# Performance work log

Hardware: AMD Instinct MI355X
Metric: run time of the kernel (lower is better)

The kernel has to match this reference:

```python
import jax, jax.numpy as jnp
import numpy as np

EMBED_DIM = 1024
N_HEADS = 16


def setup_inputs() -> dict:
    key = jax.random.key(0)
    k1, k2, k3 = jax.random.split(key, 3)
    B, T, C = 4, 2048, EMBED_DIM
    x0 = jax.random.normal(k1, (B, T, C), dtype=jnp.float32)
    # Linear weights stored as (in, out) so y = x @ W, matching torch Linear math.
    w_attn = jax.random.normal(k2, (C, 3 * C), dtype=jnp.float32) * (1.0 / np.sqrt(C))
    w_proj = jax.random.normal(k3, (C, C), dtype=jnp.float32) * (1.0 / np.sqrt(C))
    return {"x0": x0, "w_attn": w_attn, "w_proj": w_proj}


def reference(x0, w_attn, w_proj):
    B, T, C = x0.shape
    H = N_HEADS
    D = C // H  # head dim
    qkv = x0 @ w_attn                      # [B, T, 3C]
    q, k, v = jnp.split(qkv, 3, axis=-1)
    # [B, T, C] -> [B, H, T, D]
    q = q.reshape(B, T, H, D).transpose(0, 2, 1, 3)
    k = k.reshape(B, T, H, D).transpose(0, 2, 1, 3)
    v = v.reshape(B, T, H, D).transpose(0, 2, 1, 3)
    scale = 1.0 / np.sqrt(D)
    attn = jnp.einsum('bhqd,bhkd->bhqk', q, k) * scale  # [B, H, T, T]
    causal = jnp.tril(jnp.ones((T, T), dtype=bool))
    attn = jnp.where(causal[None, None, :, :], attn, -jnp.inf)
    attn = jax.nn.softmax(attn, axis=-1)
    y = jnp.einsum('bhqk,bhkd->bhqd', attn, v)           # [B, H, T, D]
    y = y.transpose(0, 2, 1, 3).reshape(B, T, C)
    return y @ w_proj
```

## Files before the change

kernel.cpp:

```cpp
#include <hip/hip_runtime.h>

#define TSEQ 2048
#define NB 4
#define NH 16
#define HD 64
#define CEMB 1024
#define MROWS (NB*TSEQ)

typedef _Float16 half8 __attribute__((ext_vector_type(8)));
typedef _Float16 half4_t __attribute__((ext_vector_type(4)));
typedef float floatx4 __attribute__((ext_vector_type(4)));

__device__ __forceinline__ floatx4 mfma16x32(half8 a, half8 b, floatx4 c) {
    return __builtin_amdgcn_mfma_f32_16x16x32_f16(a, b, c, 0, 0, 0);
}

__device__ __forceinline__ void async16(const _Float16* g, _Float16* l) {
    __builtin_amdgcn_global_load_lds((const __attribute__((address_space(1))) void*)g,
                                     (__attribute__((address_space(3))) void*)l, 16, 0, 0);
}

__global__ __launch_bounds__(256) void cvt_fp32_fp16(const float* __restrict__ in,
                                                     _Float16* __restrict__ out) {
    size_t i = ((size_t)blockIdx.x * 256 + threadIdx.x) * 8;
    float4 a = *(const float4*)(in + i);
    float4 b = *(const float4*)(in + i + 4);
    half8 h;
    h[0] = (_Float16)a.x; h[1] = (_Float16)a.y; h[2] = (_Float16)a.z; h[3] = (_Float16)a.w;
    h[4] = (_Float16)b.x; h[5] = (_Float16)b.y; h[6] = (_Float16)b.z; h[7] = (_Float16)b.w;
    *(half8*)(out + i) = h;
}

__global__ __launch_bounds__(256) void transpose_cvt(const float* __restrict__ in,
                                                     _Float16* __restrict__ out,
                                                     int R, int Ccols) {
    __shared__ float tile[32][33];
    int bx = blockIdx.x;
    int by = blockIdx.y;
    int tx = threadIdx.x, ty = threadIdx.y;
    int x = bx * 32 + tx;
#pragma unroll
    for (int i = 0; i < 32; i += 8) {
        int y = by * 32 + ty + i;
        tile[ty + i][tx] = in[(size_t)y * Ccols + x];
    }
    __syncthreads();
#pragma unroll
    for (int i = 0; i < 32; i += 8) {
        int oc = bx * 32 + ty + i;
        int orow = by * 32 + tx;
        out[(size_t)oc * R + orow] = (_Float16)tile[tx][ty + i];
    }
}

template<int MODE>
__global__ __launch_bounds__(512, 2) void gemm_nt8(const _Float16* __restrict__ A,
                                                   const _Float16* __restrict__ Bt,
                                                   float* __restrict__ Cf,
                                                   _Float16* __restrict__ Ch,
                                                   _Float16* __restrict__ VTh,
                                                   int N, int K) {
    __shared__ __align__(16) _Float16 As[4][128 * 32];
    __shared__ __align__(16) _Float16 Bs[4][256 * 32];

    const int tid = threadIdx.x;
    const int wv = tid >> 6, lane = tid & 63;
    const int wm = wv >> 2, wn = wv & 3;
    const int l16 = lane & 15, quad = lane >> 4;

    const int pid = blockIdx.x + gridDim.x * blockIdx.y;
    const int nn = gridDim.y;
    const int pig = 8 * nn;
    const int gid = pid / pig;
    const int rem = pid - gid * pig;
    const int bm = gid * 8 + (rem & 7);
    const int bn = rem >> 3;

    const int rA = tid >> 2;
    const int kA = ((tid & 3) ^ ((rA >> 1) & 3)) * 8;
    const _Float16* Ag  = A  + (size_t)(bm * 128 + rA) * K + kA;
    const _Float16* Bg0 = Bt + (size_t)(bn * 256 + rA) * K + kA;
    const _Float16* Bg1 = Bg0 + (size_t)128 * K;

    auto stage = [&](int slot, int ss) {
        async16(Ag  + ss * 32, &As[slot][wv * 512]);
        async16(Bg0 + ss * 32, &Bs[slot][wv * 512]);
        async16(Bg1 + ss * 32, &Bs[slot][4096 + wv * 512]);
    };

    const floatx4 zero = {0.f, 0.f, 0.f, 0.f};
    floatx4 acc[4][4];
#pragma unroll
    for (int i = 0; i < 4; i++)
#pragma unroll
        for (int j = 0; j < 4; j++) acc[i][j] = zero;

    const int sw2 = (quad ^ ((l16 >> 1) & 3)) * 8;
    const int offA = (wm * 64 + l16) * 32 + sw2;
    const int offB = (wn * 64 + l16) * 32 + sw2;

    stage(0, 0); stage(1, 1); stage(2, 2);
    asm volatile("s_waitcnt vmcnt(6)\n\ts_barrier" ::: "memory");

    const int NS = K >> 5;
    for (int it = 0; it < NS / 4; ++it) {
#pragma unroll
        for (int p = 0; p < 4; ++p) {
            const int s = it * 4 + p;
            half8 af[4], bf[4];
#pragma unroll
            for (int i = 0; i < 4; i++) af[i] = *(const half8*)&As[p][offA + i * 512];
#pragma unroll
            for (int j = 0; j < 4; j++) bf[j] = *(const half8*)&Bs[p][offB + j * 512];
            if (s + 3 < NS) stage((p + 3) & 3, s + 3);
            asm volatile("s_barrier" ::: "memory");
            __builtin_amdgcn_sched_barrier(0);
            __builtin_amdgcn_s_setprio(1);
#pragma unroll
            for (int i = 0; i < 4; i++)
#pragma unroll
                for (int j = 0; j < 4; j++)
                    acc[i][j] = mfma16x32(af[i], bf[j], acc[i][j]);
            __builtin_amdgcn_s_setprio(0);
            __builtin_amdgcn_sched_barrier(0);
            asm volatile("s_waitcnt vmcnt(6)\n\ts_barrier" ::: "memory");
        }
    }

    if (MODE == 1) {
#pragma unroll
        for (int i = 0; i < 4; i++) {
            int row = bm * 128 + wm * 64 + i * 16 + quad * 4;
#pragma unroll
            for (int j = 0; j < 4; j++) {
                int col = bn * 256 + wn * 64 + j * 16 + l16;
#pragma unroll
                for (int r = 0; r < 4; r++)
                    Cf[(size_t)(row + r) * N + col] = acc[i][j][r];
            }
        }
    } else {
        const int which = bn >> 2;
        if (which < 2) {
#pragma unroll
            for (int j = 0; j < 4; j++) {
                int n = bn * 256 + wn * 64 + j * 16 + l16;
                int c = n & 1023, h = c >> 6, d = c & 63;
                _Float16* dst = Ch + (size_t)which * ((size_t)MROWS * CEMB)
                                   + (size_t)h * (TSEQ * HD) + d;
#pragma unroll
                for (int i = 0; i < 4; i++) {
                    int row = bm * 128 + wm * 64 + i * 16 + quad * 4;
#pragma unroll
                    for (int r = 0; r < 4; r++) {
                        int m = row + r;
                        int b = m >> 11, t = m & 2047;
                        dst[(size_t)b * (NH * TSEQ * HD) + (size_t)t * HD] = (_Float16)acc[i][j][r];
                    }
                }
            }
        } else {
#pragma unroll
            for (int j = 0; j < 4; j++) {
                int n = bn * 256 + wn * 64 + j * 16 + l16;
                int c = n & 1023, h = c >> 6, d = c & 63;
#pragma unroll
                for (int i = 0; i < 4; i++) {
                    int m0 = bm * 128 + wm * 64 + i * 16 + quad * 4;
                    int b = m0 >> 11, t = m0 & 2047;
                    half4_t pk;
#pragma unroll
                    for (int r = 0; r < 4; r++) pk[r] = (_Float16)acc[i][j][r];
                    *(half4_t*)&VTh[(((size_t)(b * NH + h)) * HD + d) * TSEQ + t] = pk;
                }
            }
        }
    }
}

__global__ __launch_bounds__(512, 4) void attn_fwd(const _Float16* __restrict__ Qg,
                                                   const _Float16* __restrict__ Kg,
                                                   const _Float16* __restrict__ VTg,
                                                   _Float16* __restrict__ Y) {
    __shared__ __align__(16) _Float16 Ks[2][4096];
    __shared__ __align__(16) _Float16 Vt[2][4096];

    const int tid = threadIdx.x;
    const int w = tid >> 6, lane = tid & 63;
    const int l16 = lane & 15, quad = lane >> 4;
    const int bh = blockIdx.y;
    const int x = blockIdx.x;
    const int b = bh >> 4, h = bh & 15;
    const int qt = (b < 2) ? x : (7 - x);

    const _Float16* Qb = Qg + (size_t)bh * TSEQ * HD;
    const _Float16* Kb = Kg + (size_t)bh * TSEQ * HD;
    const _Float16* Vb = VTg + (size_t)bh * HD * TSEQ;

    const _Float16 ksc = (_Float16)(0.125f * 1.44269504089f);
    const floatx4 zero = {0.f, 0.f, 0.f, 0.f};

    half8 qf[2][2];
#pragma unroll
    for (int g = 0; g < 2; g++) {
        const _Float16* qrow = Qb + (size_t)(qt * 256 + g * 128 + w * 16 + l16) * HD;
        qf[g][0] = *(const half8*)(qrow + quad * 8);
        qf[g][1] = *(const half8*)(qrow + 32 + quad * 8);
#pragma unroll
        for (int e = 0; e < 8; e++) { qf[g][0][e] *= ksc; qf[g][1][e] *= ksc; }
    }

    floatx4 o[2][4];
#pragma unroll
    for (int g = 0; g < 2; g++)
#pragma unroll
        for (int dt = 0; dt < 4; dt++) o[g][dt] = zero;
    float lsum[2] = {0.f, 0.f};

    const int srow8 = lane >> 3;
    const int scol8 = ((lane & 7) ^ (lane >> 3)) * 8;

    auto stage = [&](int bf, int kt2) {
        const int row = w * 8 + srow8;
        async16(Kb + (size_t)(kt2 * 64 + row) * HD + scol8, &Ks[bf][w * 512]);
        async16(Vb + (size_t)row * TSEQ + kt2 * 64 + scol8, &Vt[bf][w * 512]);
    };

    const int kmax = 4 * qt + 3;
    stage(0, 0);
    int buf = 0;
    for (int kt = 0; kt <= kmax; ++kt) {
        __syncthreads();
        if (kt < kmax) stage(buf ^ 1, kt + 1);

        half8 kf0[4], kf1[4];
#pragma unroll
        for (int nj = 0; nj < 4; nj++) {
            const int rb = (nj * 16 + l16) * 64;
            kf0[nj] = *(const half8*)&Ks[buf][rb + ((quad ^ (l16 & 7)) * 8)];
            kf1[nj] = *(const half8*)&Ks[buf][rb + (((quad ^ 4) ^ (l16 & 7)) * 8)];
        }

        const bool doA = (kt <= 4 * qt + 1);
        half8 pf[2][2];
#pragma unroll
        for (int g = 0; g < 2; g++) {
            if (g == 0 && !doA) continue;
            floatx4 st[4];
#pragma unroll
            for (int nj = 0; nj < 4; nj++) {
                floatx4 t = mfma16x32(kf0[nj], qf[g][0], zero);
                st[nj] = mfma16x32(kf1[nj], qf[g][1], t);
            }
            if (kt * 64 + 63 > qt * 256 + g * 128 + w * 16) {
                const int klim = qt * 256 + g * 128 + w * 16 + l16 - kt * 64;
#pragma unroll
                for (int nj = 0; nj < 4; nj++)
#pragma unroll
                    for (int r = 0; r < 4; r++) {
                        int key = nj * 16 + quad * 4 + r;
                        if (key > klim) st[nj][r] = -1e30f;
                    }
            }
#pragma unroll
            for (int nj = 0; nj < 4; nj++)
#pragma unroll
                for (int r = 0; r < 4; r++) {
                    float p = __builtin_amdgcn_exp2f(st[nj][r]);
                    lsum[g] += p;
                    pf[g][nj >> 1][(nj & 1) * 4 + r] = (_Float16)p;
                }
        }

#pragma unroll
        for (int u = 0; u < 2; u++) {
#pragma unroll
            for (int dt = 0; dt < 4; dt++) {
                const int rb = (dt * 16 + l16) * 64;
                const int g0 = u * 4 + (quad >> 1);
                const int sub = (quad & 1) * 4;
                half4_t lo = *(const half4_t*)&Vt[buf][rb + ((g0 ^ (l16 & 7)) * 8 + sub)];
                half4_t hi = *(const half4_t*)&Vt[buf][rb + (((g0 + 2) ^ (l16 & 7)) * 8 + sub)];
                half8 vf;
                vf[0] = lo[0]; vf[1] = lo[1]; vf[2] = lo[2]; vf[3] = lo[3];
                vf[4] = hi[0]; vf[5] = hi[1]; vf[6] = hi[2]; vf[7] = hi[3];
                if (doA) o[0][dt] = mfma16x32(pf[0][u], vf, o[0][dt]);
                o[1][dt] = mfma16x32(pf[1][u], vf, o[1][dt]);
            }
        }
        buf ^= 1;
    }

#pragma unroll
    for (int g = 0; g < 2; g++) {
        float lt = lsum[g];
        lt += __shfl_xor(lt, 16);
        lt += __shfl_xor(lt, 32);
        float linv[4];
#pragma unroll
        for (int r = 0; r < 4; r++) linv[r] = 1.0f / __shfl(lt, quad * 4 + r);
#pragma unroll
        for (int dt = 0; dt < 4; dt++)
#pragma unroll
            for (int r = 0; r < 4; r++) {
                int q = qt * 256 + g * 128 + w * 16 + quad * 4 + r;
                int d = dt * 16 + l16;
                Y[((size_t)(b * TSEQ + q)) * CEMB + h * HD + d] = (_Float16)(o[g][dt][r] * linv[r]);
            }
    }
}

extern "C" void kernel_launch(void* const* d_in, const int* in_sizes, int n_in,
                              void* d_out, int out_size, void* d_ws, size_t ws_size,
                              hipStream_t stream) {
    const float* x0     = (const float*)d_in[0];
    const float* w_attn = (const float*)d_in[1];
    const float* w_proj = (const float*)d_in[2];
    float* out = (float*)d_out;

    _Float16* xh  = (_Float16*)d_ws;
    _Float16* wqt = xh  + (size_t)MROWS * CEMB;
    _Float16* wpt = wqt + (size_t)3 * CEMB * CEMB;
    _Float16* qh  = wpt + (size_t)CEMB * CEMB;
    _Float16* kh  = qh  + (size_t)MROWS * CEMB;
    _Float16* vt  = kh  + (size_t)MROWS * CEMB;
    _Float16* yh  = vt  + (size_t)MROWS * CEMB;

    cvt_fp32_fp16<<<(MROWS * CEMB) / (256 * 8), 256, 0, stream>>>(x0, xh);
    transpose_cvt<<<dim3(3 * CEMB / 32, CEMB / 32), dim3(32, 8), 0, stream>>>(w_attn, wqt, CEMB, 3 * CEMB);
    transpose_cvt<<<dim3(CEMB / 32, CEMB / 32), dim3(32, 8), 0, stream>>>(w_proj, wpt, CEMB, CEMB);

    gemm_nt8<0><<<dim3(MROWS / 128, 3 * CEMB / 256), 512, 0, stream>>>(xh, wqt, nullptr, qh, vt, 3 * CEMB, CEMB);
    attn_fwd<<<dim3(TSEQ / 256, NB * NH), 512, 0, stream>>>(qh, kh, vt, yh);
    gemm_nt8<1><<<dim3(MROWS / 128, CEMB / 256), 512, 0, stream>>>(yh, wpt, out, nullptr, nullptr, CEMB, CEMB);
}
```

Baseline: 242.6 us.

## Double-buffer GEMM register fragments and deepen LDS prefetch to four stages

Restructures the GEMM main loop so LDS-to-register fragment loads for the next k-step are issued before the MFMAs of the current step, using two register fragment buffers. Global-to-LDS async staging now runs four slots ahead, and one of the two barriers per step is removed. The loop trip count is hardcoded to 7 outer iterations plus an epilogue, which assumes K equals 1024. This raises register pressure and breaks if K changes. The tighter waitcnt and barrier placement needs care, because the slot being overwritten must no longer be read by other waves.

```diff
diff --git a/kernel.cpp b/kernel.cpp
--- a/kernel.cpp
+++ b/kernel.cpp
@@ -99,33 +99,49 @@
     const int offA = (wm * 64 + l16) * 32 + sw2;
     const int offB = (wn * 64 + l16) * 32 + sw2;
 
-    stage(0, 0); stage(1, 1); stage(2, 2);
+    half8 fa[2][4], fb[2][4];
+
+#define LDF(d, slot)                                                         \
+    do {                                                                     \
+        _Pragma("unroll") for (int i_ = 0; i_ < 4; i_++)                     \
+            fa[d][i_] = *(const half8*)&As[slot][offA + i_ * 512];           \
+        _Pragma("unroll") for (int j_ = 0; j_ < 4; j_++)                     \
+            fb[d][j_] = *(const half8*)&Bs[slot][offB + j_ * 512];           \
+    } while (0)
+
+#define MM(d)                                                                \
+    do {                                                                     \
+        __builtin_amdgcn_s_setprio(1);                                       \
+        _Pragma("unroll") for (int i_ = 0; i_ < 4; i_++)                     \
+            _Pragma("unroll") for (int j_ = 0; j_ < 4; j_++)                 \
+                acc[i_][j_] = mfma16x32(fa[d][i_], fb[d][j_], acc[i_][j_]);  \
+        __builtin_amdgcn_s_setprio(0);                                       \
+    } while (0)
+
+    stage(0, 0); stage(1, 1); stage(2, 2); stage(3, 3);
     asm volatile("s_waitcnt vmcnt(6)\n\ts_barrier" ::: "memory");
-
-    const int NS = K >> 5;
-    for (int it = 0; it < NS / 4; ++it) {
+    LDF(0, 0);
+
+    for (int it = 0; it < 7; ++it) {
 #pragma unroll
         for (int p = 0; p < 4; ++p) {
-            const int s = it * 4 + p;
-            half8 af[4], bf[4];
-#pragma unroll
-            for (int i = 0; i < 4; i++) af[i] = *(const half8*)&As[p][offA + i * 512];
-#pragma unroll
-            for (int j = 0; j < 4; j++) bf[j] = *(const half8*)&Bs[p][offB + j * 512];
-            if (s + 3 < NS) stage((p + 3) & 3, s + 3);
-            asm volatile("s_barrier" ::: "memory");
+            stage(p, it * 4 + p + 4);
+            LDF((p & 1) ^ 1, (p + 1) & 3);
+            MM(p & 1);
+            asm volatile("s_waitcnt vmcnt(6) lgkmcnt(0)\n\ts_barrier" ::: "memory");
             __builtin_amdgcn_sched_barrier(0);
-            __builtin_amdgcn_s_setprio(1);
-#pragma unroll
-            for (int i = 0; i < 4; i++)
-#pragma unroll
-                for (int j = 0; j < 4; j++)
-                    acc[i][j] = mfma16x32(af[i], bf[j], acc[i][j]);
-            __builtin_amdgcn_s_setprio(0);
-            __builtin_amdgcn_sched_barrier(0);
-            asm volatile("s_waitcnt vmcnt(6)\n\ts_barrier" ::: "memory");
-        }
-    }
+        }
+    }
+    LDF(1, 1); MM(0);
+    asm volatile("s_waitcnt vmcnt(3)\n\ts_barrier" ::: "memory");
+    __builtin_amdgcn_sched_barrier(0);
+    LDF(0, 2); MM(1);
+    asm volatile("s_waitcnt vmcnt(0)\n\ts_barrier" ::: "memory");
+    __builtin_amdgcn_sched_barrier(0);
+    LDF(1, 3); MM(0);
+    MM(1);
+#undef LDF
+#undef MM
 
     if (MODE == 1) {
 #pragma unroll
```

Result: slower. 249.9 us (+3.0%).

## Restructure GEMM to 4 waves with 128x64 per-wave tiles and 3-stage pipeline

Applied to the files above, without the earlier changes.

The GEMM kernel now runs with 256 threads (4 waves) instead of 512. Each wave computes a full 128-row by 64-column output tile (8x4 MFMA accumulators), so each A fragment is reused across more MFMAs. The LDS ring drops from 4 to 3 stages, with a fully unrolled loop hardcoded for K=1024 (32 k-steps), and one barrier per phase instead of two. This raises register pressure and ties the kernel to K=1024.

```diff
diff --git a/kernel.cpp b/kernel.cpp
--- a/kernel.cpp
+++ b/kernel.cpp
@@ -54,18 +54,17 @@
 }
 
 template<int MODE>
-__global__ __launch_bounds__(512, 2) void gemm_nt8(const _Float16* __restrict__ A,
-                                                   const _Float16* __restrict__ Bt,
-                                                   float* __restrict__ Cf,
-                                                   _Float16* __restrict__ Ch,
-                                                   _Float16* __restrict__ VTh,
-                                                   int N, int K) {
-    __shared__ __align__(16) _Float16 As[4][128 * 32];
-    __shared__ __align__(16) _Float16 Bs[4][256 * 32];
+__global__ __launch_bounds__(256, 2) void gemm_w4(const _Float16* __restrict__ A,
+                                                  const _Float16* __restrict__ Bt,
+                                                  float* __restrict__ Cf,
+                                                  _Float16* __restrict__ Ch,
+                                                  _Float16* __restrict__ VTh,
+                                                  int N, int K) {
+    __shared__ __align__(16) _Float16 As[3][128 * 32];
+    __shared__ __align__(16) _Float16 Bs[3][256 * 32];
 
     const int tid = threadIdx.x;
     const int wv = tid >> 6, lane = tid & 63;
-    const int wm = wv >> 2, wn = wv & 3;
     const int l16 = lane & 15, quad = lane >> 4;
 
     const int pid = blockIdx.x + gridDim.x * blockIdx.y;
@@ -77,63 +76,71 @@
     const int bn = rem >> 3;
 
     const int rA = tid >> 2;
-    const int kA = ((tid & 3) ^ ((rA >> 1) & 3)) * 8;
-    const _Float16* Ag  = A  + (size_t)(bm * 128 + rA) * K + kA;
-    const _Float16* Bg0 = Bt + (size_t)(bn * 256 + rA) * K + kA;
-    const _Float16* Bg1 = Bg0 + (size_t)128 * K;
+    const int kA = ((tid & 3) ^ ((tid >> 3) & 3)) * 8;
+    const _Float16* Ag = A  + (size_t)(bm * 128 + rA) * K + kA;
+    const _Float16* Bg = Bt + (size_t)(bn * 256 + rA) * K + kA;
 
     auto stage = [&](int slot, int ss) {
-        async16(Ag  + ss * 32, &As[slot][wv * 512]);
-        async16(Bg0 + ss * 32, &Bs[slot][wv * 512]);
-        async16(Bg1 + ss * 32, &Bs[slot][4096 + wv * 512]);
+        const int k0 = ss * 32;
+#pragma unroll
+        for (int u = 0; u < 2; u++)
+            async16(Ag + (size_t)(u * 64) * K + k0, &As[slot][tid * 8 + u * 2048]);
+#pragma unroll
+        for (int u = 0; u < 4; u++)
+            async16(Bg + (size_t)(u * 64) * K + k0, &Bs[slot][tid * 8 + u * 2048]);
     };
 
     const floatx4 zero = {0.f, 0.f, 0.f, 0.f};
-    floatx4 acc[4][4];
-#pragma unroll
-    for (int i = 0; i < 4; i++)
+    floatx4 acc[8][4];
+#pragma unroll
+    for (int i = 0; i < 8; i++)
 #pragma unroll
         for (int j = 0; j < 4; j++) acc[i][j] = zero;
 
     const int sw2 = (quad ^ ((l16 >> 1) & 3)) * 8;
-    const int offA = (wm * 64 + l16) * 32 + sw2;
-    const int offB = (wn * 64 + l16) * 32 + sw2;
+    const int offA = l16 * 32 + sw2;
+    const int offB = (wv * 64 + l16) * 32 + sw2;
+
+#define PHASE(s, slot, slot2, STG, WAIT)                                        \
+    do {                                                                        \
+        if (STG) stage(slot2, (s) + 2);                                         \
+        half8 af[8], bf[4];                                                     \
+        _Pragma("unroll") for (int i_ = 0; i_ < 8; i_++)                        \
+            af[i_] = *(const half8*)&As[slot][offA + i_ * 512];                 \
+        _Pragma("unroll") for (int j_ = 0; j_ < 4; j_++)                        \
+            bf[j_] = *(const half8*)&Bs[slot][offB + j_ * 512];                 \
+        __builtin_amdgcn_s_setprio(1);                                          \
+        _Pragma("unroll") for (int i_ = 0; i_ < 8; i_++)                        \
+            _Pragma("unroll") for (int j_ = 0; j_ < 4; j_++)                    \
+                acc[i_][j_] = mfma16x32(af[i_], bf[j_], acc[i_][j_]);           \
+        __builtin_amdgcn_s_setprio(0);                                          \
+        if (WAIT == 2)                                                          \
+            asm volatile("s_waitcnt vmcnt(6) lgkmcnt(0)\n\ts_barrier" ::: "memory"); \
+        else if (WAIT == 1)                                                     \
+            asm volatile("s_waitcnt vmcnt(0) lgkmcnt(0)\n\ts_barrier" ::: "memory"); \
+        __builtin_amdgcn_sched_barrier(0);                                      \
+    } while (0)
 
     stage(0, 0); stage(1, 1); stage(2, 2);
-    asm volatile("s_waitcnt vmcnt(6)\n\ts_barrier" ::: "memory");
-
-    const int NS = K >> 5;
-    for (int it = 0; it < NS / 4; ++it) {
-#pragma unroll
-        for (int p = 0; p < 4; ++p) {
-            const int s = it * 4 + p;
-            half8 af[4], bf[4];
-#pragma unroll
-            for (int i = 0; i < 4; i++) af[i] = *(const half8*)&As[p][offA + i * 512];
-#pragma unroll
-            for (int j = 0; j < 4; j++) bf[j] = *(const half8*)&Bs[p][offB + j * 512];
-            if (s + 3 < NS) stage((p + 3) & 3, s + 3);
-            asm volatile("s_barrier" ::: "memory");
-            __builtin_amdgcn_sched_barrier(0);
-            __builtin_amdgcn_s_setprio(1);
-#pragma unroll
-            for (int i = 0; i < 4; i++)
-#pragma unroll
-                for (int j = 0; j < 4; j++)
-                    acc[i][j] = mfma16x32(af[i], bf[j], acc[i][j]);
-            __builtin_amdgcn_s_setprio(0);
-            __builtin_amdgcn_sched_barrier(0);
-            asm volatile("s_waitcnt vmcnt(6)\n\ts_barrier" ::: "memory");
-        }
-    }
+    asm volatile("s_waitcnt vmcnt(12)\n\ts_barrier" ::: "memory");
+
+    for (int it = 0; it < 10; ++it) {
+        const int s0 = it * 3;
+        PHASE(s0 + 0, 0, 2, 1, 2);
+        PHASE(s0 + 1, 1, 0, 1, 2);
+        PHASE(s0 + 2, 2, 1, 1, 2);
+    }
+    PHASE(30, 0, 0, 0, 1);
+    PHASE(31, 1, 0, 0, 0);
+#undef PHASE
 
     if (MODE == 1) {
 #pragma unroll
-        for (int i = 0; i < 4; i++) {
-            int row = bm * 128 + wm * 64 + i * 16 + quad * 4;
+        for (int i = 0; i < 8; i++) {
+            int row = bm * 128 + i * 16 + quad * 4;
 #pragma unroll
             for (int j = 0; j < 4; j++) {
-                int col = bn * 256 + wn * 64 + j * 16 + l16;
+                int col = bn * 256 + wv * 64 + j * 16 + l16;
 #pragma unroll
                 for (int r = 0; r < 4; r++)
                     Cf[(size_t)(row + r) * N + col] = acc[i][j][r];
@@ -144,13 +151,13 @@
         if (which < 2) {
 #pragma unroll
             for (int j = 0; j < 4; j++) {
-                int n = bn * 256 + wn * 64 + j * 16 + l16;
+                int n = bn * 256 + wv * 64 + j * 16 + l16;
                 int c = n & 1023, h = c >> 6, d = c & 63;
                 _Float16* dst = Ch + (size_t)which * ((size_t)MROWS * CEMB)
                                    + (size_t)h * (TSEQ * HD) + d;
 #pragma unroll
-                for (int i = 0; i < 4; i++) {
-                    int row = bm * 128 + wm * 64 + i * 16 + quad * 4;
+                for (int i = 0; i < 8; i++) {
+                    int row = bm * 128 + i * 16 + quad * 4;
 #pragma unroll
                     for (int r = 0; r < 4; r++) {
                         int m = row + r;
@@ -162,11 +169,11 @@
         } else {
 #pragma unroll
             for (int j = 0; j < 4; j++) {
-                int n = bn * 256 + wn * 64 + j * 16 + l16;
+                int n = bn * 256 + wv * 64 + j * 16 + l16;
                 int c = n & 1023, h = c >> 6, d = c & 63;
 #pragma unroll
-                for (int i = 0; i < 4; i++) {
-                    int m0 = bm * 128 + wm * 64 + i * 16 + quad * 4;
+                for (int i = 0; i < 8; i++) {
+                    int m0 = bm * 128 + i * 16 + quad * 4;
                     int b = m0 >> 11, t = m0 & 2047;
                     half4_t pk;
 #pragma unroll
@@ -330,7 +337,7 @@
     transpose_cvt<<<dim3(3 * CEMB / 32, CEMB / 32), dim3(32, 8), 0, stream>>>(w_attn, wqt, CEMB, 3 * CEMB);
     transpose_cvt<<<dim3(CEMB / 32, CEMB / 32), dim3(32, 8), 0, stream>>>(w_proj, wpt, CEMB, CEMB);
 
-    gemm_nt8<0><<<dim3(MROWS / 128, 3 * CEMB / 256), 512, 0, stream>>>(xh, wqt, nullptr, qh, vt, 3 * CEMB, CEMB);
+    gemm_w4<0><<<dim3(MROWS / 128, 3 * CEMB / 256), 256, 0, stream>>>(xh, wqt, nullptr, qh, vt, 3 * CEMB, CEMB);
     attn_fwd<<<dim3(TSEQ / 256, NB * NH), 512, 0, stream>>>(qh, kh, vt, yh);
-    gemm_nt8<1><<<dim3(MROWS / 128, CEMB / 256), 512, 0, stream>>>(yh, wpt, out, nullptr, nullptr, CEMB, CEMB);
-}
+    gemm_w4<1><<<dim3(MROWS / 128, CEMB / 256), 256, 0, stream>>>(yh, wpt, out, nullptr, nullptr, CEMB, CEMB);
+}
```

After: 245.9 us. Within noise of the previous version (+1.4%).
